# Kernel optimization log

Measured on AMD Instinct MI355X. Metric: run time of the kernel, lower is better.

## Reference

```python
import jax, jax.numpy as jnp
import numpy as np

ALPHA, BETA, GAMMA = 0.05, 0.95, 0.95   # list_weight
TANH_ALPHA = 2.0
GDEP = 2


def _gcn_rnn(x, adp, preA, W, b):
    # GCN type 'RNN': adaptive batched adj + predefined adj
    h = x
    outs = [h]
    for _ in range(GDEP):
        h = (ALPHA * x
             + BETA * jnp.einsum('nvc,nvw->nwc', h, adp)
             + GAMMA * jnp.einsum('nvc,vw->nwc', h, preA))
        outs.append(h)
    return jnp.concatenate(outs, -1) @ W + b


def _gcn_hyper(x, A, W, b):
    h = x
    outs = [h]
    for _ in range(GDEP):
        h = ALPHA * x + GAMMA * jnp.einsum('nvc,vw->nwc', h, A)
        outs.append(h)
    return jnp.concatenate(outs, -1) @ W + b


def _gcn_tgn(x, Ab, W, b):
    h = x
    outs = [h]
    for _ in range(GDEP):
        h = ALPHA * x + GAMMA * jnp.einsum('nvc,nvw->nwc', h, Ab)
        outs.append(h)
    return jnp.concatenate(outs, -1) @ W + b


def setup_inputs() -> dict:
    key = jax.random.key(0)
    ks = jax.random.split(key, 28)
    B, T, N, F = 16, 24, 512, 2
    H, E = 64, 16          # hidden_size, node embedding dim (dims_hyper[-1])
    TGN_OUT = 32
    D_ATTN = 4 * F         # TAttn default dim_out = 4 * dim_in
    p = lambda i, shape: jax.random.normal(ks[i], shape, dtype=jnp.float32) * 0.1
    return {
        'sample': jax.random.normal(ks[0], (B, T, N, F), dtype=jnp.float32),
        'predefined_A': jax.random.uniform(ks[1], (N, N), dtype=jnp.float32),
        'w_query': p(2, (F, D_ATTN)), 'w_key': p(3, (F, D_ATTN)),
        'attn_bias': p(4, (D_ATTN,)), 'attn_trans': p(5, (D_ATTN, 1)),
        'W_tgn': p(6, ((GDEP + 1) * F, TGN_OUT)), 'b_tgn': p(7, (TGN_OUT,)),
        'W_agg1': p(8, ((GDEP + 1) * H, E)), 'b_agg1': p(9, (E,)),
        'W_agg2': p(10, ((GDEP + 1) * H, E)), 'b_agg2': p(11, (E,)),
        'W_srcemb': p(12, (F, E)), 'b_srcemb': p(13, (E,)),
        'W_tgtemb': p(14, (F, E)), 'b_tgtemb': p(15, (E,)),
        'W_gz': p(16, ((GDEP + 1) * (F + H), H)), 'b_gz': p(17, (H,)),
        'W_gr': p(18, ((GDEP + 1) * (F + H), H)), 'b_gr': p(19, (H,)),
        'W_gc': p(20, ((GDEP + 1) * (F + H), H)), 'b_gc': p(21, (H,)),
        'W_short': p(22, (TGN_OUT, F)), 'b_short': p(23, (F,)),
        'W_long': p(24, (H, F)), 'b_long': p(25, (F,)),
        'W_mix': p(26, (TGN_OUT + H, F)), 'b_mix': p(27, (F,)),
    }


def reference(sample, predefined_A, w_query, w_key, attn_bias, attn_trans,
              W_tgn, b_tgn, W_agg1, b_agg1, W_agg2, b_agg2,
              W_srcemb, b_srcemb, W_tgtemb, b_tgtemb,
              W_gz, b_gz, W_gr, b_gr, W_gc, b_gc,
              W_short, b_short, W_long, b_long, W_mix, b_mix):
    B, T, N, F = sample.shape
    H = W_long.shape[0]
    A = predefined_A
    eye = jnp.eye(N, dtype=sample.dtype)

    def gru_step(hidden, graph):
        # hidden: [B,N,H], graph: [B,N,F]
        gs = _gcn_hyper(hidden, A, W_agg1, b_agg1)
        gt = _gcn_hyper(hidden, A, W_agg2, b_agg2)
        nv_s = jnp.tanh(TANH_ALPHA * (graph @ W_srcemb + b_srcemb) * gs)
        nv_t = jnp.tanh(TANH_ALPHA * (graph @ W_tgtemb + b_tgtemb) * gt)
        a = (jnp.einsum('bnd,bmd->bnm', nv_s, nv_t)
             - jnp.einsum('bnd,bmd->bnm', nv_t, nv_s))
        adp = jax.nn.relu(jnp.tanh(TANH_ALPHA * a)) + eye
        adp = adp / adp.sum(-1, keepdims=True)           # row-normalized [B,N,N]
        combined = jnp.concatenate([graph, hidden], -1)
        z = jax.nn.sigmoid(_gcn_rnn(combined, adp, A, W_gz, b_gz))
        r = jax.nn.sigmoid(_gcn_rnn(combined, adp, A, W_gr, b_gr))
        c = jnp.tanh(_gcn_rnn(jnp.concatenate([graph, r * hidden], -1), adp, A, W_gc, b_gc))
        return z * hidden + (1.0 - z) * c

    hidden = jnp.zeros((B, N, H), dtype=sample.dtype)
    graphs = jnp.moveaxis(sample[:, 0:T - 4:4], 1, 0)    # [T', B, N, F]
    hidden = jax.lax.scan(lambda h, g: (gru_step(h, g), None), hidden, graphs)[0]

    # temporal additive attention over the last 4 graphs (TAttn)
    src = sample[:, -4:]                                  # [B,4,N,F]
    tar = sample[:, -1]                                   # [B,N,F]
    q = (tar @ w_query)[:, None, :, None, :]              # [B,1,N,1,D]
    k = (src @ w_key)[:, :, None, :, :]                   # [B,4,1,N,D]
    scores = (jnp.tanh(q + k + attn_bias) @ attn_trans)[..., 0]   # [B,4,N,N]
    attn = jax.nn.softmax(scores, axis=-1)

    # single TGN layer: graph conv with (predefined + attention) adjacency
    Ab = A[None] + attn.reshape(-1, N, N)                 # [B*4,N,N]
    out = _gcn_tgn(src.reshape(-1, N, F), Ab, W_tgn, b_tgn)
    out = jax.nn.relu(out.reshape(B, 4, N, -1))
    tar = out.sum(axis=1)                                 # [B,N,TGN_OUT]

    gat_result = tar @ W_short + b_short                  # [B,N,F]
    hidden = gru_step(hidden, gat_result)
    gru_result = hidden @ W_long + b_long
    final_result = jnp.concatenate([tar, hidden], -1) @ W_mix + b_mix
    return gat_result, gru_result, final_result, attn
```

## Files before the change

### kernel.cpp

```cpp
#include <hip/hip_runtime.h>

#define ALPHA_C 0.05f
#define BETA_C  0.95f
#define GAMMA_C 0.95f

constexpr int B = 16, T = 24, N = 512, F = 2, H = 64, E = 16;
constexpr int DA = 8;
constexpr int CC = F + H;
constexpr int TGN_OC = 32;
constexpr int NPART = 4;

__device__ __forceinline__ float fast_rcp(float x) { return __builtin_amdgcn_rcpf(x); }
__device__ __forceinline__ float fast_tanh(float x) {
    return 1.0f - 2.0f * fast_rcp(__expf(2.0f * x) + 1.0f);
}
__device__ __forceinline__ float fast_sigmoid(float x) {
    return fast_rcp(1.0f + __expf(-x));
}

__global__ void scaleA_kernel(const float* __restrict__ A, float* __restrict__ K1)
{
    int i = blockIdx.x * 256 + threadIdx.x;
    K1[i] = GAMMA_C * A[i];
}

__global__ __launch_bounds__(256) void k2_kernel(const float* __restrict__ A,
                                                 float* __restrict__ K2)
{
    __shared__ float rows[16][258];
    __shared__ float cols[256][17];
    const int tid = threadIdx.x;
    const int r0 = blockIdx.y * 16, c0 = blockIdx.x * 16;
    const int rr = tid >> 4, cc = tid & 15;
    float acc = 0.f;
    for (int k0 = 0; k0 < N; k0 += 256) {
#pragma unroll
        for (int it = 0; it < 4; ++it) {
            int l = it * 256 + tid;
            int row = l >> 6, k4 = (l & 63) << 2;
            *(float4*)&rows[row][k4] = *(const float4*)(A + (size_t)(r0 + row) * N + k0 + k4);
        }
#pragma unroll
        for (int it = 0; it < 4; ++it) {
            int l = it * 256 + tid;
            int k = l >> 2, c4 = (l & 3) << 2;
            *(float4*)&cols[k][c4] = *(const float4*)(A + (size_t)(k0 + k) * N + c0 + c4);
        }
        __syncthreads();
#pragma unroll 8
        for (int k = 0; k < 256; ++k) acc += rows[rr][k] * cols[k][cc];
        __syncthreads();
    }
    size_t i = (size_t)(r0 + rr) * N + c0 + cc;
    K2[i] = GAMMA_C * ALPHA_C * A[i] + GAMMA_C * GAMMA_C * acc;
}

template<int GCOLS, bool INSUM, bool MPB>
__device__ __forceinline__ void bmm_core(
    float* __restrict__ out, const float* __restrict__ x, const float* __restrict__ in,
    const float* __restrict__ M, int b, int w0, int vq, int tid,
    float (*sh_m)[68], float (*sh_h)[68])
{
    constexpr int Crow = 64 + GCOLS;
    const size_t pstr = (size_t)B * N * Crow;
    const int cg = tid & 15;
    const int wg = tid >> 4;

    float acc[2][4] = {{0,0,0,0},{0,0,0,0}};
    float ag[2] = {0.f, 0.f};

    const float* Mb = M + (MPB ? (size_t)b * N * N : 0);
    const float* inb = in + (size_t)b * N * Crow;

    for (int vt = 0; vt < 2; ++vt) {
        const int v0 = vq * 128 + vt * 64;
#pragma unroll
        for (int it = 0; it < 2; ++it) {
            int l = it * 512 + tid;
            int row = l >> 4, c4 = (l & 15) << 2;
            *(float4*)&sh_m[row][c4] =
                *(const float4*)(Mb + (size_t)(v0 + row) * N + w0 + c4);
        }
        if (GCOLS == 2) {
            const float2* h0 = (const float2*)(inb + (size_t)v0 * Crow);
            for (int l = tid; l < 64 * 33; l += 512) {
                int row = l / 33, k = (l - row * 33) * 2;
                float2 v = h0[l];
                if (INSUM) {
#pragma unroll
                    for (int j = 1; j < NPART; ++j) {
                        float2 w = ((const float2*)(inb + (size_t)j * pstr + (size_t)v0 * Crow))[l];
                        v.x += w.x; v.y += w.y;
                    }
                }
                *(float2*)&sh_h[row][k] = v;
            }
        } else {
            const float4* h0 = (const float4*)(inb + (size_t)v0 * Crow);
#pragma unroll
            for (int it = 0; it < 2; ++it) {
                int l = it * 512 + tid;
                int row = l >> 4, k = (l & 15) << 2;
                float4 v = h0[l];
                if (INSUM) {
#pragma unroll
                    for (int j = 1; j < NPART; ++j) {
                        float4 w = ((const float4*)(inb + (size_t)j * pstr + (size_t)v0 * Crow))[l];
                        v.x += w.x; v.y += w.y; v.z += w.z; v.w += w.w;
                    }
                }
                *(float4*)&sh_h[row][k] = v;
            }
        }
        __syncthreads();
#pragma unroll 8
        for (int j = 0; j < 64; ++j) {
            float2 mv = *(const float2*)&sh_m[j][wg << 1];
            float4 hv = *(const float4*)&sh_h[j][cg << 2];
            acc[0][0] += mv.x * hv.x; acc[0][1] += mv.x * hv.y;
            acc[0][2] += mv.x * hv.z; acc[0][3] += mv.x * hv.w;
            acc[1][0] += mv.y * hv.x; acc[1][1] += mv.y * hv.y;
            acc[1][2] += mv.y * hv.z; acc[1][3] += mv.y * hv.w;
            if (GCOLS > 0 && cg < GCOLS) {
                float gv = sh_h[j][64 + cg];
                ag[0] += mv.x * gv; ag[1] += mv.y * gv;
            }
        }
        __syncthreads();
    }
    float* outp = out + (size_t)vq * pstr + (size_t)b * N * Crow;
    const float* xb = x + (size_t)b * N * Crow;
#pragma unroll
    for (int r = 0; r < 2; ++r) {
        const int w = w0 + (wg << 1) + r;
        const size_t base = (size_t)w * Crow + (cg << 2);
        if (GCOLS == 2) {
            float o0 = acc[r][0], o1 = acc[r][1], o2 = acc[r][2], o3 = acc[r][3];
            if (vq == 0) {
                o0 += ALPHA_C * xb[base];     o1 += ALPHA_C * xb[base + 1];
                o2 += ALPHA_C * xb[base + 2]; o3 += ALPHA_C * xb[base + 3];
            }
            float2 lo = {o0, o1}, hi = {o2, o3};
            *(float2*)(outp + base) = lo;
            *(float2*)(outp + base + 2) = hi;
            if (cg < GCOLS) {
                size_t gb = (size_t)w * Crow + 64 + cg;
                float v = ag[r];
                if (vq == 0) v += ALPHA_C * xb[gb];
                outp[gb] = v;
            }
        } else {
            float4 ov = {acc[r][0], acc[r][1], acc[r][2], acc[r][3]};
            if (vq == 0) {
                float4 xv = *(const float4*)(xb + base);
                ov.x += ALPHA_C * xv.x; ov.y += ALPHA_C * xv.y;
                ov.z += ALPHA_C * xv.z; ov.w += ALPHA_C * xv.w;
            }
            *(float4*)(outp + base) = ov;
        }
    }
}

template<bool INSUM>
__global__ __launch_bounds__(512) void bmm4_kernel(
    float* __restrict__ out, const float* __restrict__ x, const float* __restrict__ in,
    const float* __restrict__ M)
{
    __shared__ float sh_m[64][68];
    __shared__ float sh_h[64][68];
    bmm_core<2, INSUM, true>(out, x, in, M, blockIdx.z, blockIdx.x * 64, blockIdx.y,
                             threadIdx.x, sh_m, sh_h);
}

__global__ __launch_bounds__(512) void hyper_kernel(
    float* __restrict__ P1, float* __restrict__ P2, const float* __restrict__ hidden,
    const float* __restrict__ K1, const float* __restrict__ K2)
{
    __shared__ float sh_m[64][68];
    __shared__ float sh_h[64][68];
    int vq = blockIdx.y & 3, which = blockIdx.y >> 2;
    float* out = which ? P2 : P1;
    const float* M = which ? K2 : K1;
    bmm_core<0, false, false>(out, hidden, hidden, M, blockIdx.z, blockIdx.x * 64, vq,
                              threadIdx.x, sh_m, sh_h);
}

__global__ __launch_bounds__(256) void gsgt4_kernel(
    const float* __restrict__ hidden, const float* __restrict__ P1, const float* __restrict__ P2,
    const float* __restrict__ Wa1, const float* __restrict__ ba1,
    const float* __restrict__ Wa2, const float* __restrict__ ba2,
    const float* __restrict__ graph, long gstride,
    const float* __restrict__ Wsrc, const float* __restrict__ bsrc,
    const float* __restrict__ Wtgt, const float* __restrict__ btgt,
    float* __restrict__ nv_s, float* __restrict__ nv_t)
{
    constexpr size_t psH = (size_t)B * N * H;
    __shared__ float sh[16][194];
    const int tid = threadIdx.x;
    const int e = tid & 15;
    const int row = tid >> 4;
    const size_t nn0 = (size_t)blockIdx.x * 16;
    {
        int f4 = ((int)(nn0) + row) * 16 + e;
        float4 v = ((const float4*)hidden)[f4];
        *(float4*)&sh[row][e << 2] = v;
        float4 a = ((const float4*)P1)[f4];
#pragma unroll
        for (int j = 1; j < NPART; ++j) {
            float4 w = ((const float4*)(P1 + (size_t)j * psH))[f4];
            a.x += w.x; a.y += w.y; a.z += w.z; a.w += w.w;
        }
        *(float4*)&sh[row][64 + (e << 2)] = a;
        float4 c = ((const float4*)P2)[f4];
#pragma unroll
        for (int j = 1; j < NPART; ++j) {
            float4 w = ((const float4*)(P2 + (size_t)j * psH))[f4];
            c.x += w.x; c.y += w.y; c.z += w.z; c.w += w.w;
        }
        *(float4*)&sh[row][128 + (e << 2)] = c;
    }
    __syncthreads();
    float gs = ba1[e], gt = ba2[e];
#pragma unroll 4
    for (int sk = 0; sk < 192; ++sk) {
        float v = sh[row][sk];
        gs += v * Wa1[(size_t)sk * E + e];
        gt += v * Wa2[(size_t)sk * E + e];
    }
    size_t nn = nn0 + row;
    int b = (int)(nn >> 9), n = (int)(nn & (N - 1));
    const float* g = graph + (size_t)b * gstride + (size_t)n * F;
    float g0 = g[0], g1 = g[1];
    float es = g0 * Wsrc[e] + g1 * Wsrc[E + e] + bsrc[e];
    float et = g0 * Wtgt[e] + g1 * Wtgt[E + e] + btgt[e];
    nv_s[nn * E + e] = fast_tanh(2.0f * es * gs);
    nv_t[nn * E + e] = fast_tanh(2.0f * et * gt);
}

__global__ __launch_bounds__(512) void adp3_kernel(
    const float* __restrict__ nv_s, const float* __restrict__ nv_t,
    const float* __restrict__ A,
    const float* __restrict__ hidden, const float* __restrict__ graph, long gstride,
    float* __restrict__ Mcomb, float* __restrict__ comb)
{
    __shared__ float red[8][4];
    __shared__ float tot[4];
    const int m = threadIdx.x;
    const int n0 = blockIdx.x * 4;
    const int b = blockIdx.y;
    const float4* sm = (const float4*)(nv_s + ((size_t)b * N + m) * E);
    const float4* tm = (const float4*)(nv_t + ((size_t)b * N + m) * E);
    const float4* sn = (const float4*)(nv_s + ((size_t)b * N + n0) * E);
    const float4* tn = (const float4*)(nv_t + ((size_t)b * N + n0) * E);
    float a1[4] = {0.f,0.f,0.f,0.f}, a2[4] = {0.f,0.f,0.f,0.f};
#pragma unroll
    for (int dd = 0; dd < 4; ++dd) {
        float4 smv = sm[dd], tmv = tm[dd];
#pragma unroll
        for (int r = 0; r < 4; ++r) {
            float4 snv = sn[r * 4 + dd], tnv = tn[r * 4 + dd];
            a1[r] += snv.x * tmv.x + snv.y * tmv.y + snv.z * tmv.z + snv.w * tmv.w;
            a2[r] += tnv.x * smv.x + tnv.y * smv.y + tnv.z * smv.z + tnv.w * smv.w;
        }
    }
    float p[4];
#pragma unroll
    for (int r = 0; r < 4; ++r) {
        float pv = fmaxf(fast_tanh(2.0f * (a1[r] - a2[r])), 0.0f);
        if (m == n0 + r) pv += 1.0f;
        p[r] = pv;
    }
    float sr[4] = {p[0], p[1], p[2], p[3]};
    for (int o = 32; o > 0; o >>= 1) {
#pragma unroll
        for (int r = 0; r < 4; ++r) sr[r] += __shfl_down(sr[r], o);
    }
    int wid = m >> 6, lane = m & 63;
    if (lane == 0) {
#pragma unroll
        for (int r = 0; r < 4; ++r) red[wid][r] = sr[r];
    }
    __syncthreads();
    if (m < 4) {
        float t = 0.f;
        for (int i = 0; i < 8; ++i) t += red[i][m];
        tot[m] = BETA_C * fast_rcp(t);
    }
    __syncthreads();
#pragma unroll
    for (int r = 0; r < 4; ++r)
        Mcomb[((size_t)b * N + n0 + r) * N + m] =
            GAMMA_C * A[(size_t)(n0 + r) * N + m] + p[r] * tot[r];
    if (m < 4 * CC) {
        int r = m / CC, k = m - r * CC;
        size_t nn = (size_t)b * N + n0 + r;
        float v;
        if (k < F) v = graph[(size_t)b * gstride + (size_t)(n0 + r) * F + k];
        else       v = hidden[nn * H + (k - F)];
        comb[nn * CC + k] = v;
    }
}

__device__ __forceinline__ void stage_rnn4(float (*sh)[200], const float* base,
                                           const float* P1, const float* P2,
                                           size_t nn0, int tid)
{
    constexpr size_t psC = (size_t)B * N * CC;
    const float2* c2 = (const float2*)(base + nn0 * CC);
    for (int l = tid; l < 16 * 33; l += 256) {
        int row = l / 33, k = (l - row * 33) * 2;
        *(float2*)&sh[row][k] = c2[l];
        float2 a = ((const float2*)(P1 + nn0 * CC))[l];
#pragma unroll
        for (int j = 1; j < NPART; ++j) {
            float2 w = ((const float2*)(P1 + (size_t)j * psC + nn0 * CC))[l];
            a.x += w.x; a.y += w.y;
        }
        *(float2*)&sh[row][66 + k] = a;
        float2 c = ((const float2*)(P2 + nn0 * CC))[l];
#pragma unroll
        for (int j = 1; j < NPART; ++j) {
            float2 w = ((const float2*)(P2 + (size_t)j * psC + nn0 * CC))[l];
            c.x += w.x; c.y += w.y;
        }
        *(float2*)&sh[row][132 + k] = c;
    }
    __syncthreads();
}

__global__ __launch_bounds__(256) void zr4_kernel(
    const float* __restrict__ comb, const float* __restrict__ P1, const float* __restrict__ P2,
    const float* __restrict__ Wgz, const float* __restrict__ bgz,
    const float* __restrict__ Wgr, const float* __restrict__ bgr,
    const float* __restrict__ hidden,
    float* __restrict__ z, float* __restrict__ comb2)
{
    __shared__ float sh[16][200];
    const int tid = threadIdx.x;
    const int oc = tid & 63;
    const int rg = tid >> 6;
    const size_t nn0 = (size_t)blockIdx.x * 16;
    stage_rnn4(sh, comb, P1, P2, nn0, tid);
    float accz[4], accr[4];
#pragma unroll
    for (int rr = 0; rr < 4; ++rr) { accz[rr] = bgz[oc]; accr[rr] = bgr[oc]; }
#pragma unroll 2
    for (int sk = 0; sk < 198; ++sk) {
        float wz = Wgz[(size_t)sk * H + oc];
        float wr = Wgr[(size_t)sk * H + oc];
#pragma unroll
        for (int rr = 0; rr < 4; ++rr) {
            float v = sh[rg * 4 + rr][sk];
            accz[rr] += v * wz; accr[rr] += v * wr;
        }
    }
#pragma unroll
    for (int rr = 0; rr < 4; ++rr) {
        int row = rg * 4 + rr;
        size_t nn = nn0 + row;
        float zv = fast_sigmoid(accz[rr]);
        float rv = fast_sigmoid(accr[rr]);
        z[nn * H + oc] = zv;
        comb2[nn * CC + F + oc] = rv * hidden[nn * H + oc];
        if (oc < F) comb2[nn * CC + oc] = sh[row][oc];
    }
}

__global__ __launch_bounds__(256) void cup4_kernel(
    const float* __restrict__ comb2, const float* __restrict__ P1, const float* __restrict__ P2,
    const float* __restrict__ Wgc, const float* __restrict__ bgc,
    const float* __restrict__ z, float* __restrict__ hidden)
{
    __shared__ float sh[16][200];
    const int tid = threadIdx.x;
    const int oc = tid & 63;
    const int rg = tid >> 6;
    const size_t nn0 = (size_t)blockIdx.x * 16;
    stage_rnn4(sh, comb2, P1, P2, nn0, tid);
    float acc[4];
#pragma unroll
    for (int rr = 0; rr < 4; ++rr) acc[rr] = bgc[oc];
#pragma unroll 2
    for (int sk = 0; sk < 198; ++sk) {
        float wc = Wgc[(size_t)sk * H + oc];
#pragma unroll
        for (int rr = 0; rr < 4; ++rr) acc[rr] += sh[rg * 4 + rr][sk] * wc;
    }
#pragma unroll
    for (int rr = 0; rr < 4; ++rr) {
        size_t nn = nn0 + rg * 4 + rr;
        float cv = fast_tanh(acc[rr]);
        float zv = z[nn * H + oc];
        float ho = hidden[nn * H + oc];
        hidden[nn * H + oc] = zv * ho + (1.0f - zv) * cv;
    }
}

__global__ void qk_kernel(const float* __restrict__ sample,
                          const float* __restrict__ wq, const float* __restrict__ wk,
                          const float* __restrict__ attn_bias,
                          float* __restrict__ q, float* __restrict__ kk)
{
    int idx = blockIdx.x * 256 + threadIdx.x;
    if (idx < B * N * DA) {
        int d = idx & 7;
        int n = (idx >> 3) & (N - 1);
        int b = idx >> 12;
        const float* tar = sample + (((size_t)b * T + (T - 1)) * N + n) * F;
        q[idx] = tar[0] * wq[d] + tar[1] * wq[DA + d] + attn_bias[d];
    } else {
        int j = idx - B * N * DA;
        int d = j & 7;
        int n = (j >> 3) & (N - 1);
        int t = (j >> 12) & 3;
        int b = j >> 14;
        const float* s = sample + (((size_t)b * T + (T - 4 + t)) * N + n) * F;
        kk[j] = s[0] * wk[d] + s[1] * wk[DA + d];
    }
}

__global__ __launch_bounds__(256) void scores3_kernel(
    const float* __restrict__ q, const float* __restrict__ kk,
    const float* __restrict__ trans, float* __restrict__ attn)
{
    int bt = blockIdx.y;
    int b = bt >> 2;
    int rbase = blockIdx.x * 16;
    int wid = threadIdx.x >> 6, lane = threadIdx.x & 63;
    const float* kkbt = kk + (size_t)bt * N * DA;
    float* attnbt = attn + (size_t)bt * N * N;
    float tr[8];
#pragma unroll
    for (int d = 0; d < 8; ++d) tr[d] = trans[d];
    for (int i = 0; i < 4; ++i) {
        int n = rbase + wid * 4 + i;
        const float* qp = q + ((size_t)b * N + n) * DA;
        float4 qa = *(const float4*)qp, qb = *(const float4*)(qp + 4);
        float ev[8]; float ssum = 0.f;
#pragma unroll
        for (int k = 0; k < 8; ++k) {
            const float* kp = kkbt + (size_t)(k * 64 + lane) * DA;
            float4 ka = *(const float4*)kp, kb = *(const float4*)(kp + 4);
            float s = fast_tanh(qa.x + ka.x) * tr[0] + fast_tanh(qa.y + ka.y) * tr[1]
                    + fast_tanh(qa.z + ka.z) * tr[2] + fast_tanh(qa.w + ka.w) * tr[3]
                    + fast_tanh(qb.x + kb.x) * tr[4] + fast_tanh(qb.y + kb.y) * tr[5]
                    + fast_tanh(qb.z + kb.z) * tr[6] + fast_tanh(qb.w + kb.w) * tr[7];
            ev[k] = __expf(s);
            ssum += ev[k];
        }
        for (int o = 32; o > 0; o >>= 1) ssum += __shfl_down(ssum, o);
        ssum = __shfl(ssum, 0);
        float rinv = fast_rcp(ssum);
#pragma unroll
        for (int k = 0; k < 8; ++k)
            attnbt[(size_t)n * N + k * 64 + lane] = ev[k] * rinv;
    }
}

__global__ __launch_bounds__(256) void tgn2_kernel(
    const float* __restrict__ A, const float* __restrict__ attn,
    const float* __restrict__ hbase, long hsB, long hsT,
    const float* __restrict__ xbase, long xsB, long xsT,
    float* __restrict__ out)
{
    __shared__ float sh_m[64][65];
    __shared__ float sh_h[64][2];
    int bt = blockIdx.y;
    int w0 = blockIdx.x * 64;
    int tid = threadIdx.x;
    int wl = tid >> 2, c = tid & 1, vh = (tid >> 1) & 1;
    const float* hp = hbase + (size_t)(bt >> 2) * hsB + (size_t)(bt & 3) * hsT;
    const float* ap = attn + (size_t)bt * N * N;
    float acc = 0.f;
    for (int vt = 0; vt < 8; ++vt) {
        int v0 = vt * 64;
#pragma unroll
        for (int it = 0; it < 16; ++it) {
            int l = it * 256 + tid;
            int vr = l >> 6, wc = l & 63;
            size_t gi = (size_t)(v0 + vr) * N + (w0 + wc);
            sh_m[wc][vr] = A[gi] + ap[gi];
        }
        if (tid < 128) sh_h[tid >> 1][tid & 1] = hp[(size_t)(v0 + (tid >> 1)) * F + (tid & 1)];
        __syncthreads();
#pragma unroll
        for (int jj = 0; jj < 32; ++jj) {
            int j = vh * 32 + jj;
            acc += sh_m[wl][j] * sh_h[j][c];
        }
        __syncthreads();
    }
    acc += __shfl_xor(acc, 2);
    if (vh == 0) {
        const float* xp = xbase + (size_t)(bt >> 2) * xsB + (size_t)(bt & 3) * xsT;
        out[((size_t)bt * N + w0 + wl) * F + c] =
            ALPHA_C * xp[(size_t)(w0 + wl) * F + c] + GAMMA_C * acc;
    }
}

__global__ __launch_bounds__(256) void tgn_out_gat_kernel(
    const float* __restrict__ sample,
    const float* __restrict__ th1, const float* __restrict__ th2,
    const float* __restrict__ Wt, const float* __restrict__ bt_,
    const float* __restrict__ Ws, const float* __restrict__ bs,
    float* __restrict__ tar32, float* __restrict__ out0)
{
    __shared__ float sh_t[8][33];
    const int tid = threadIdx.x;
    const int oc = tid & 31;
    const int r = tid >> 5;
    const size_t nn = (size_t)blockIdx.x * 8 + r;
    const int n = (int)(nn & (N - 1));
    const int b = (int)(nn >> 9);
    float acc = 0.f;
    for (int t = 0; t < 4; ++t) {
        int bt = b * 4 + t;
        const float* s = sample + (((size_t)b * T + (T - 4 + t)) * N + n) * F;
        size_t rr = ((size_t)bt * N + n) * F;
        float v = bt_[oc];
        v += s[0] * Wt[0 * TGN_OC + oc] + s[1] * Wt[1 * TGN_OC + oc];
        v += th1[rr] * Wt[2 * TGN_OC + oc] + th1[rr + 1] * Wt[3 * TGN_OC + oc];
        v += th2[rr] * Wt[4 * TGN_OC + oc] + th2[rr + 1] * Wt[5 * TGN_OC + oc];
        acc += fmaxf(v, 0.0f);
    }
    tar32[nn * TGN_OC + oc] = acc;
    sh_t[r][oc] = acc;
    __syncthreads();
    if (tid < 16) {
        int row = tid >> 1, f = tid & 1;
        size_t nn2 = (size_t)blockIdx.x * 8 + row;
        float g = bs[f];
#pragma unroll
        for (int k = 0; k < TGN_OC; ++k) g += sh_t[row][k] * Ws[(size_t)k * F + f];
        out0[nn2 * F + f] = g;
    }
}

__global__ void final_kernel(const float* __restrict__ hidden, const float* __restrict__ tar32,
                             const float* __restrict__ Wl, const float* __restrict__ bl,
                             const float* __restrict__ Wm, const float* __restrict__ bm,
                             float* __restrict__ dout_gru, float* __restrict__ dout_fin)
{
    int idx = blockIdx.x * 256 + threadIdx.x;
    int f = idx & 1;
    int nn = idx >> 1;
    const float* hp = hidden + (size_t)nn * H;
    const float* tp = tar32 + (size_t)nn * TGN_OC;
    float g = bl[f], fin = bm[f];
    for (int k = 0; k < H; ++k) g += hp[k] * Wl[(size_t)k * F + f];
    for (int k = 0; k < TGN_OC; ++k) fin += tp[k] * Wm[(size_t)k * F + f];
    for (int k = 0; k < H; ++k) fin += hp[k] * Wm[(size_t)(TGN_OC + k) * F + f];
    dout_gru[idx] = g;
    dout_fin[idx] = fin;
}

namespace {
struct Ptrs {
    const float *sample, *A, *wq, *wk, *attn_bias, *attn_trans, *Wt, *bt_;
    const float *Wa1, *ba1, *Wa2, *ba2, *Wsrc, *bsrc, *Wtgt, *btgt;
    const float *Wgz, *bgz, *Wgr, *bgr, *Wgc, *bgc, *Wsh, *bsh, *Wl, *bl, *Wm, *bm;
    float *hidden, *nvs, *nvt, *Mcomb, *K1, *K2, *comb, *comb2, *z, *P1, *P2;
    float *q, *kk, *th1, *th2, *tar32;
};

void gru_step(hipStream_t stream, const Ptrs& p, const float* graph, long gstride)
{
    dim3 bg(8, NPART, B);
    hyper_kernel<<<dim3(8, 2 * NPART, B), 512, 0, stream>>>(p.P1, p.P2, p.hidden, p.K1, p.K2);
    gsgt4_kernel<<<B * N / 16, 256, 0, stream>>>(
        p.hidden, p.P1, p.P2, p.Wa1, p.ba1, p.Wa2, p.ba2, graph, gstride,
        p.Wsrc, p.bsrc, p.Wtgt, p.btgt, p.nvs, p.nvt);
    adp3_kernel<<<dim3(N / 4, B), 512, 0, stream>>>(
        p.nvs, p.nvt, p.A, p.hidden, graph, gstride, p.Mcomb, p.comb);
    bmm4_kernel<false><<<bg, 512, 0, stream>>>(p.P1, p.comb, p.comb, p.Mcomb);
    bmm4_kernel<true><<<bg, 512, 0, stream>>>(p.P2, p.comb, p.P1, p.Mcomb);
    zr4_kernel<<<B * N / 16, 256, 0, stream>>>(
        p.comb, p.P1, p.P2, p.Wgz, p.bgz, p.Wgr, p.bgr, p.hidden, p.z, p.comb2);
    bmm4_kernel<false><<<bg, 512, 0, stream>>>(p.P1, p.comb2, p.comb2, p.Mcomb);
    bmm4_kernel<true><<<bg, 512, 0, stream>>>(p.P2, p.comb2, p.P1, p.Mcomb);
    cup4_kernel<<<B * N / 16, 256, 0, stream>>>(
        p.comb2, p.P1, p.P2, p.Wgc, p.bgc, p.z, p.hidden);
}
}

extern "C" void kernel_launch(void* const* d_in, const int* in_sizes, int n_in,
                              void* d_out, int out_size, void* d_ws, size_t ws_size,
                              hipStream_t stream)
{
    (void)in_sizes; (void)n_in; (void)out_size; (void)ws_size;
    Ptrs p;
    p.sample = (const float*)d_in[0];
    p.A      = (const float*)d_in[1];
    p.wq     = (const float*)d_in[2];
    p.wk     = (const float*)d_in[3];
    p.attn_bias  = (const float*)d_in[4];
    p.attn_trans = (const float*)d_in[5];
    p.Wt  = (const float*)d_in[6];
    p.bt_ = (const float*)d_in[7];
    p.Wa1 = (const float*)d_in[8];
    p.ba1 = (const float*)d_in[9];
    p.Wa2 = (const float*)d_in[10];
    p.ba2 = (const float*)d_in[11];
    p.Wsrc = (const float*)d_in[12];
    p.bsrc = (const float*)d_in[13];
    p.Wtgt = (const float*)d_in[14];
    p.btgt = (const float*)d_in[15];
    p.Wgz = (const float*)d_in[16];
    p.bgz = (const float*)d_in[17];
    p.Wgr = (const float*)d_in[18];
    p.bgr = (const float*)d_in[19];
    p.Wgc = (const float*)d_in[20];
    p.bgc = (const float*)d_in[21];
    p.Wsh = (const float*)d_in[22];
    p.bsh = (const float*)d_in[23];
    p.Wl  = (const float*)d_in[24];
    p.bl  = (const float*)d_in[25];
    p.Wm  = (const float*)d_in[26];
    p.bm  = (const float*)d_in[27];

    float* ws = (float*)d_ws;
    size_t off = 0;
    auto alloc = [&](size_t nelem) { float* r = ws + off; off += nelem; return r; };
    p.hidden = alloc((size_t)B * N * H);
    p.nvs    = alloc((size_t)B * N * E);
    p.nvt    = alloc((size_t)B * N * E);
    p.Mcomb  = alloc((size_t)B * N * N);
    p.K1     = alloc((size_t)N * N);
    p.K2     = alloc((size_t)N * N);
    p.comb   = alloc((size_t)B * N * CC);
    p.comb2  = alloc((size_t)B * N * CC);
    p.z      = alloc((size_t)B * N * H);
    p.P1     = alloc((size_t)NPART * B * N * CC);
    p.P2     = alloc((size_t)NPART * B * N * CC);
    p.q      = alloc((size_t)B * N * DA);
    p.kk     = alloc((size_t)B * 4 * N * DA);
    p.th1    = alloc((size_t)B * 4 * N * F);
    p.th2    = alloc((size_t)B * 4 * N * F);
    p.tar32  = alloc((size_t)B * N * TGN_OC);

    float* out = (float*)d_out;
    float* out_gat = out;
    float* out_gru = out + (size_t)B * N * F;
    float* out_fin = out + (size_t)2 * B * N * F;
    float* out_attn = out + (size_t)3 * B * N * F;

    hipMemsetAsync(p.hidden, 0, (size_t)B * N * H * sizeof(float), stream);
    scaleA_kernel<<<N * N / 256, 256, 0, stream>>>(p.A, p.K1);
    k2_kernel<<<dim3(32, 32), 256, 0, stream>>>(p.A, p.K2);

    for (int i = 0; i < 5; ++i) {
        const float* graph = p.sample + (size_t)(4 * i) * N * F;
        gru_step(stream, p, graph, (long)T * N * F);
    }

    qk_kernel<<<(B * N * DA + B * 4 * N * DA) / 256, 256, 0, stream>>>(
        p.sample, p.wq, p.wk, p.attn_bias, p.q, p.kk);
    scores3_kernel<<<dim3(32, 64), 256, 0, stream>>>(p.q, p.kk, p.attn_trans, out_attn);

    const float* srcbase = p.sample + (size_t)(T - 4) * N * F;
    tgn2_kernel<<<dim3(8, 64), 256, 0, stream>>>(
        p.A, out_attn, srcbase, (long)T * N * F, (long)N * F,
        srcbase, (long)T * N * F, (long)N * F, p.th1);
    tgn2_kernel<<<dim3(8, 64), 256, 0, stream>>>(
        p.A, out_attn, p.th1, (long)4 * N * F, (long)N * F,
        srcbase, (long)T * N * F, (long)N * F, p.th2);
    tgn_out_gat_kernel<<<B * N / 8, 256, 0, stream>>>(
        p.sample, p.th1, p.th2, p.Wt, p.bt_, p.Wsh, p.bsh, p.tar32, out_gat);

    gru_step(stream, p, out_gat, (long)N * F);

    final_kernel<<<(B * N * F) / 256, 256, 0, stream>>>(
        p.hidden, p.tar32, p.Wl, p.bl, p.Wm, p.bm, out_gru, out_fin);
}
```

Measured before the change: 1.523 ms.

## Stage gate weights in LDS and register-tile GRU gate matmuls

The gsgt kernel now loads the aggregation weights into shared memory transposed, so the dot products use float4 LDS reads instead of strided global loads. The zr and cup gate kernels store the activations transposed, stage weight chunks in LDS in three 66-row pieces, and give each thread a 4x2 or 2x2 output tile, which raises FMA reuse per load. zr now splits z and r outputs across thread halves. The cost is extra barriers and more shared memory per block, which may lower occupancy.

```diff
diff --git a/kernel.cpp b/kernel.cpp
--- a/kernel.cpp
+++ b/kernel.cpp
@@ -185,7 +185,7 @@
                               threadIdx.x, sh_m, sh_h);
 }
 
-__global__ __launch_bounds__(256) void gsgt4_kernel(
+__global__ __launch_bounds__(256) void gsgt5_kernel(
     const float* __restrict__ hidden, const float* __restrict__ P1, const float* __restrict__ P2,
     const float* __restrict__ Wa1, const float* __restrict__ ba1,
     const float* __restrict__ Wa2, const float* __restrict__ ba2,
@@ -195,7 +195,9 @@
     float* __restrict__ nv_s, float* __restrict__ nv_t)
 {
     constexpr size_t psH = (size_t)B * N * H;
-    __shared__ float sh[16][194];
+    __shared__ float sh[16][196];
+    __shared__ float W1t[16][196];
+    __shared__ float W2t[16][196];
     const int tid = threadIdx.x;
     const int e = tid & 15;
     const int row = tid >> 4;
@@ -219,13 +221,24 @@
         }
         *(float4*)&sh[row][128 + (e << 2)] = c;
     }
+    for (int l = tid; l < 768; l += 256) {
+        int sk = l >> 2, q = l & 3;
+        float4 w1 = ((const float4*)Wa1)[l];
+        float4 w2 = ((const float4*)Wa2)[l];
+        W1t[4 * q + 0][sk] = w1.x; W1t[4 * q + 1][sk] = w1.y;
+        W1t[4 * q + 2][sk] = w1.z; W1t[4 * q + 3][sk] = w1.w;
+        W2t[4 * q + 0][sk] = w2.x; W2t[4 * q + 1][sk] = w2.y;
+        W2t[4 * q + 2][sk] = w2.z; W2t[4 * q + 3][sk] = w2.w;
+    }
     __syncthreads();
     float gs = ba1[e], gt = ba2[e];
-#pragma unroll 4
-    for (int sk = 0; sk < 192; ++sk) {
-        float v = sh[row][sk];
-        gs += v * Wa1[(size_t)sk * E + e];
-        gt += v * Wa2[(size_t)sk * E + e];
+#pragma unroll 8
+    for (int sk = 0; sk < 192; sk += 4) {
+        float4 xv = *(const float4*)&sh[row][sk];
+        float4 w1 = *(const float4*)&W1t[e][sk];
+        float4 w2 = *(const float4*)&W2t[e][sk];
+        gs += xv.x * w1.x + xv.y * w1.y + xv.z * w1.z + xv.w * w1.w;
+        gt += xv.x * w2.x + xv.y * w2.y + xv.z * w2.z + xv.w * w2.w;
     }
     size_t nn = nn0 + row;
     int b = (int)(nn >> 9), n = (int)(nn & (N - 1));
@@ -301,98 +314,152 @@
     }
 }
 
-__device__ __forceinline__ void stage_rnn4(float (*sh)[200], const float* base,
-                                           const float* P1, const float* P2,
-                                           size_t nn0, int tid)
+__device__ __forceinline__ void stage_xt(float (*Xt)[20], const float* __restrict__ base,
+                                         const float* __restrict__ P1,
+                                         const float* __restrict__ P2,
+                                         size_t nn0, int tid)
 {
     constexpr size_t psC = (size_t)B * N * CC;
     const float2* c2 = (const float2*)(base + nn0 * CC);
+    const float2* p1b = (const float2*)(P1 + nn0 * CC);
+    const float2* p2b = (const float2*)(P2 + nn0 * CC);
     for (int l = tid; l < 16 * 33; l += 256) {
-        int row = l / 33, k = (l - row * 33) * 2;
-        *(float2*)&sh[row][k] = c2[l];
-        float2 a = ((const float2*)(P1 + nn0 * CC))[l];
+        int row = l & 15, kp = l >> 4;
+        int idx = row * 33 + kp;
+        float2 v = c2[idx];
+        Xt[2 * kp][row] = v.x; Xt[2 * kp + 1][row] = v.y;
+        float2 a = p1b[idx];
 #pragma unroll
         for (int j = 1; j < NPART; ++j) {
-            float2 w = ((const float2*)(P1 + (size_t)j * psC + nn0 * CC))[l];
+            float2 w = ((const float2*)(P1 + (size_t)j * psC + nn0 * CC))[idx];
             a.x += w.x; a.y += w.y;
         }
-        *(float2*)&sh[row][66 + k] = a;
-        float2 c = ((const float2*)(P2 + nn0 * CC))[l];
+        Xt[66 + 2 * kp][row] = a.x; Xt[66 + 2 * kp + 1][row] = a.y;
+        float2 c = p2b[idx];
 #pragma unroll
         for (int j = 1; j < NPART; ++j) {
-            float2 w = ((const float2*)(P2 + (size_t)j * psC + nn0 * CC))[l];
+            float2 w = ((const float2*)(P2 + (size_t)j * psC + nn0 * CC))[idx];
             c.x += w.x; c.y += w.y;
         }
-        *(float2*)&sh[row][132 + k] = c;
-    }
-    __syncthreads();
-}
-
-__global__ __launch_bounds__(256) void zr4_kernel(
+        Xt[132 + 2 * kp][row] = c.x; Xt[132 + 2 * kp + 1][row] = c.y;
+    }
+}
+
+__global__ __launch_bounds__(256) void zr5_kernel(
     const float* __restrict__ comb, const float* __restrict__ P1, const float* __restrict__ P2,
     const float* __restrict__ Wgz, const float* __restrict__ bgz,
     const float* __restrict__ Wgr, const float* __restrict__ bgr,
     const float* __restrict__ hidden,
     float* __restrict__ z, float* __restrict__ comb2)
 {
-    __shared__ float sh[16][200];
+    __shared__ float Xt[198][20];
+    __shared__ float Wl[66][128];
     const int tid = threadIdx.x;
-    const int oc = tid & 63;
+    const size_t nn0 = (size_t)blockIdx.x * 16;
+
+    stage_xt(Xt, comb, P1, P2, nn0, tid);
+
+    const int cp = tid & 63;
     const int rg = tid >> 6;
-    const size_t nn0 = (size_t)blockIdx.x * 16;
-    stage_rnn4(sh, comb, P1, P2, nn0, tid);
-    float accz[4], accr[4];
-#pragma unroll
-    for (int rr = 0; rr < 4; ++rr) { accz[rr] = bgz[oc]; accr[rr] = bgr[oc]; }
-#pragma unroll 2
-    for (int sk = 0; sk < 198; ++sk) {
-        float wz = Wgz[(size_t)sk * H + oc];
-        float wr = Wgr[(size_t)sk * H + oc];
-#pragma unroll
-        for (int rr = 0; rr < 4; ++rr) {
-            float v = sh[rg * 4 + rr][sk];
-            accz[rr] += v * wz; accr[rr] += v * wr;
-        }
-    }
-#pragma unroll
-    for (int rr = 0; rr < 4; ++rr) {
-        int row = rg * 4 + rr;
-        size_t nn = nn0 + row;
-        float zv = fast_sigmoid(accz[rr]);
-        float rv = fast_sigmoid(accr[rr]);
-        z[nn * H + oc] = zv;
-        comb2[nn * CC + F + oc] = rv * hidden[nn * H + oc];
-        if (oc < F) comb2[nn * CC + oc] = sh[row][oc];
-    }
-}
-
-__global__ __launch_bounds__(256) void cup4_kernel(
+    float2 bias = (cp < 32) ? *(const float2*)&bgz[2 * cp]
+                            : *(const float2*)&bgr[2 * cp - 64];
+    float acc[4][2];
+#pragma unroll
+    for (int r = 0; r < 4; ++r) { acc[r][0] = bias.x; acc[r][1] = bias.y; }
+
+    for (int ch = 0; ch < 3; ++ch) {
+        const int sk0 = ch * 66;
+        for (int l = tid; l < 66 * 32; l += 256) {
+            int j = l >> 5, q = l & 31;
+            float4 w = (q < 16)
+                ? ((const float4*)(Wgz + (size_t)(sk0 + j) * H))[q]
+                : ((const float4*)(Wgr + (size_t)(sk0 + j) * H))[q - 16];
+            *(float4*)&Wl[j][q << 2] = w;
+        }
+        __syncthreads();
+#pragma unroll 6
+        for (int j = 0; j < 66; ++j) {
+            float4 xv = *(const float4*)&Xt[sk0 + j][rg << 2];
+            float2 wv = *(const float2*)&Wl[j][cp << 1];
+            acc[0][0] += xv.x * wv.x; acc[0][1] += xv.x * wv.y;
+            acc[1][0] += xv.y * wv.x; acc[1][1] += xv.y * wv.y;
+            acc[2][0] += xv.z * wv.x; acc[2][1] += xv.z * wv.y;
+            acc[3][0] += xv.w * wv.x; acc[3][1] += xv.w * wv.y;
+        }
+        __syncthreads();
+    }
+
+    if (cp < 32) {
+        const int oc = 2 * cp;
+#pragma unroll
+        for (int r = 0; r < 4; ++r) {
+            size_t nn = nn0 + (rg << 2) + r;
+            z[nn * H + oc]     = fast_sigmoid(acc[r][0]);
+            z[nn * H + oc + 1] = fast_sigmoid(acc[r][1]);
+        }
+    } else {
+        const int oc = 2 * cp - 64;
+#pragma unroll
+        for (int r = 0; r < 4; ++r) {
+            size_t nn = nn0 + (rg << 2) + r;
+            float h0 = hidden[nn * H + oc], h1 = hidden[nn * H + oc + 1];
+            comb2[nn * CC + F + oc]     = fast_sigmoid(acc[r][0]) * h0;
+            comb2[nn * CC + F + oc + 1] = fast_sigmoid(acc[r][1]) * h1;
+        }
+    }
+    if (tid < 32) {
+        int row = tid >> 1, f = tid & 1;
+        comb2[(nn0 + row) * CC + f] = Xt[f][row];
+    }
+}
+
+__global__ __launch_bounds__(256) void cup5_kernel(
     const float* __restrict__ comb2, const float* __restrict__ P1, const float* __restrict__ P2,
     const float* __restrict__ Wgc, const float* __restrict__ bgc,
     const float* __restrict__ z, float* __restrict__ hidden)
 {
-    __shared__ float sh[16][200];
+    __shared__ float Xt[198][20];
+    __shared__ float Wl[66][64];
     const int tid = threadIdx.x;
-    const int oc = tid & 63;
-    const int rg = tid >> 6;
     const size_t nn0 = (size_t)blockIdx.x * 16;
-    stage_rnn4(sh, comb2, P1, P2, nn0, tid);
-    float acc[4];
-#pragma unroll
-    for (int rr = 0; rr < 4; ++rr) acc[rr] = bgc[oc];
-#pragma unroll 2
-    for (int sk = 0; sk < 198; ++sk) {
-        float wc = Wgc[(size_t)sk * H + oc];
-#pragma unroll
-        for (int rr = 0; rr < 4; ++rr) acc[rr] += sh[rg * 4 + rr][sk] * wc;
-    }
-#pragma unroll
-    for (int rr = 0; rr < 4; ++rr) {
-        size_t nn = nn0 + rg * 4 + rr;
-        float cv = fast_tanh(acc[rr]);
-        float zv = z[nn * H + oc];
-        float ho = hidden[nn * H + oc];
-        hidden[nn * H + oc] = zv * ho + (1.0f - zv) * cv;
+
+    stage_xt(Xt, comb2, P1, P2, nn0, tid);
+
+    const int cp = tid & 31;
+    const int rg = tid >> 5;
+    float2 bias = *(const float2*)&bgc[2 * cp];
+    float acc[2][2];
+#pragma unroll
+    for (int r = 0; r < 2; ++r) { acc[r][0] = bias.x; acc[r][1] = bias.y; }
+
+    for (int ch = 0; ch < 3; ++ch) {
+        const int sk0 = ch * 66;
+        for (int l = tid; l < 66 * 16; l += 256) {
+            int j = l >> 4, q = l & 15;
+            float4 w = ((const float4*)(Wgc + (size_t)(sk0 + j) * H))[q];
+            *(float4*)&Wl[j][q << 2] = w;
+        }
+        __syncthreads();
+#pragma unroll 6
+        for (int j = 0; j < 66; ++j) {
+            float2 xv = *(const float2*)&Xt[sk0 + j][rg << 1];
+            float2 wv = *(const float2*)&Wl[j][cp << 1];
+            acc[0][0] += xv.x * wv.x; acc[0][1] += xv.x * wv.y;
+            acc[1][0] += xv.y * wv.x; acc[1][1] += xv.y * wv.y;
+        }
+        __syncthreads();
+    }
+
+    const int oc = 2 * cp;
+#pragma unroll
+    for (int r = 0; r < 2; ++r) {
+        size_t nn = nn0 + (rg << 1) + r;
+        float cv0 = fast_tanh(acc[r][0]);
+        float cv1 = fast_tanh(acc[r][1]);
+        float zv0 = z[nn * H + oc],     ho0 = hidden[nn * H + oc];
+        float zv1 = z[nn * H + oc + 1], ho1 = hidden[nn * H + oc + 1];
+        hidden[nn * H + oc]     = zv0 * ho0 + (1.0f - zv0) * cv0;
+        hidden[nn * H + oc + 1] = zv1 * ho1 + (1.0f - zv1) * cv1;
     }
 }
 
@@ -567,18 +634,18 @@
 {
     dim3 bg(8, NPART, B);
     hyper_kernel<<<dim3(8, 2 * NPART, B), 512, 0, stream>>>(p.P1, p.P2, p.hidden, p.K1, p.K2);
-    gsgt4_kernel<<<B * N / 16, 256, 0, stream>>>(
+    gsgt5_kernel<<<B * N / 16, 256, 0, stream>>>(
         p.hidden, p.P1, p.P2, p.Wa1, p.ba1, p.Wa2, p.ba2, graph, gstride,
         p.Wsrc, p.bsrc, p.Wtgt, p.btgt, p.nvs, p.nvt);
     adp3_kernel<<<dim3(N / 4, B), 512, 0, stream>>>(
         p.nvs, p.nvt, p.A, p.hidden, graph, gstride, p.Mcomb, p.comb);
     bmm4_kernel<false><<<bg, 512, 0, stream>>>(p.P1, p.comb, p.comb, p.Mcomb);
     bmm4_kernel<true><<<bg, 512, 0, stream>>>(p.P2, p.comb, p.P1, p.Mcomb);
-    zr4_kernel<<<B * N / 16, 256, 0, stream>>>(
+    zr5_kernel<<<B * N / 16, 256, 0, stream>>>(
         p.comb, p.P1, p.P2, p.Wgz, p.bgz, p.Wgr, p.bgr, p.hidden, p.z, p.comb2);
     bmm4_kernel<false><<<bg, 512, 0, stream>>>(p.P1, p.comb2, p.comb2, p.Mcomb);
     bmm4_kernel<true><<<bg, 512, 0, stream>>>(p.P2, p.comb2, p.P1, p.Mcomb);
-    cup4_kernel<<<B * N / 16, 256, 0, stream>>>(
+    cup5_kernel<<<B * N / 16, 256, 0, stream>>>(
         p.comb2, p.P1, p.P2, p.Wgc, p.bgc, p.z, p.hidden);
 }
 }
```

Measured after the change: 1.270 ms. 1.2x faster.
